# Performance work log

Measured on AMD Instinct MI355X. Metric: run time of the kernel, lower is better.

The kernel has to match this reference:

```python
import jax, jax.numpy as jnp
import numpy as np

M, D, H, E = 4096, 2048, 2048, 8


def q8(t):
    # Emulate fp8 e4m3 quantize->dequantize (DeepGEMM inputs); scale is all-ones in the source.
    return t.astype(jnp.float8_e4m3fn).astype(jnp.float32)


def setup_inputs() -> dict:
    key = jax.random.key(0)
    k1, k2, k3 = jax.random.split(key, 3)
    x = jax.random.normal(k1, (M, D), dtype=jnp.float32)
    gate_w = jax.random.normal(k2, (E, D), dtype=jnp.float32) * (D ** -0.5)
    gate_b = jnp.zeros((E,), dtype=jnp.float32)
    expert_w = jax.random.normal(k3, (E, H, D), dtype=jnp.float32) * (D ** -0.5)
    return {"x": x, "gate_w": gate_w, "gate_b": gate_b, "expert_w": expert_w}


def reference(x, gate_w, gate_b, expert_w):
    # Gating: softmax over experts. [M, E]
    gate_scores = jax.nn.softmax(x @ gate_w.T + gate_b, axis=-1)
    # fp8 quantize-dequantize of activations and expert weights (rhs_scale == 1).
    x_q = q8(x)                      # [M, D]
    w_q = q8(expert_w)               # [E, H, D]
    # Grouped GEMM (every expert applied to every token), bf16 output like deep_gemm.
    y = jnp.einsum("md,ehd->emh", x_q, w_q).astype(jnp.bfloat16)  # [E, M, H]
    # Weighted combine: sum_e gate[m,e] * y[e,m,h]
    out = jnp.einsum("me,emh->mh", gate_scores, y.astype(jnp.float32))  # [M, H]
    return out
```

## Files before the change

kernel.cpp:

```cpp
#include <hip/hip_runtime.h>
#include <hip/hip_bf16.h>

#define MDIM 4096
#define DDIM 2048
#define HDIM 2048
#define EDIM 8
#define HD   ((size_t)HDIM * DDIM)

typedef float v4f __attribute__((ext_vector_type(4)));
typedef int   v4i __attribute__((ext_vector_type(4)));
typedef int   v8i __attribute__((ext_vector_type(8)));

__device__ __forceinline__ void gl2lds16(const void* g, void* l) {
  __builtin_amdgcn_global_load_lds(
      (const __attribute__((address_space(1))) void*)g,
      (__attribute__((address_space(3))) void*)l,
      16, 0, 0);
}

__global__ __launch_bounds__(256) void k_quant(
    const float* __restrict__ x, const float* __restrict__ gw,
    const float* __restrict__ gb, const float* __restrict__ w,
    float* __restrict__ gate, unsigned char* __restrict__ x8,
    unsigned char* __restrict__ w8)
{
  if (blockIdx.x < 1024) {
    const int wid  = threadIdx.x >> 6;
    const int lane = threadIdx.x & 63;
    const int m    = blockIdx.x * 4 + wid;

    const float4* xr = (const float4*)(x + (size_t)m * DDIM);
    unsigned int* qr = (unsigned int*)(x8 + (size_t)m * DDIM);

    float part[EDIM];
#pragma unroll
    for (int e = 0; e < EDIM; ++e) part[e] = 0.f;

#pragma unroll
    for (int it = 0; it < DDIM / 4 / 64; ++it) {
      const int idx = it * 64 + lane;
      const float4 xv = xr[idx];
      int pk = __builtin_amdgcn_cvt_pk_fp8_f32(xv.x, xv.y, 0, false);
      pk = __builtin_amdgcn_cvt_pk_fp8_f32(xv.z, xv.w, pk, true);
      qr[idx] = (unsigned int)pk;
#pragma unroll
      for (int e = 0; e < EDIM; ++e) {
        const float4 wv = ((const float4*)(gw + (size_t)e * DDIM))[idx];
        part[e] += xv.x * wv.x + xv.y * wv.y + xv.z * wv.z + xv.w * wv.w;
      }
    }
#pragma unroll
    for (int e = 0; e < EDIM; ++e) {
#pragma unroll
      for (int off = 32; off > 0; off >>= 1)
        part[e] += __shfl_xor(part[e], off);
    }
    float lg[EDIM];
    float s = 0.f;
#pragma unroll
    for (int e = 0; e < EDIM; ++e) lg[e] = part[e] + gb[e];
    float mx = lg[0];
#pragma unroll
    for (int e = 1; e < EDIM; ++e) mx = fmaxf(mx, lg[e]);
#pragma unroll
    for (int e = 0; e < EDIM; ++e) { lg[e] = expf(lg[e] - mx); s += lg[e]; }
    const float inv = 1.f / s;
    if (lane < EDIM) gate[m * EDIM + lane] = lg[lane] * inv;
  } else {
    const long long n4 = (long long)EDIM * HDIM * DDIM / 4;
    const long long stride = (long long)4096 * 256;
    for (long long i = (long long)(blockIdx.x - 1024) * 256 + threadIdx.x;
         i < n4; i += stride) {
      const float4 v = ((const float4*)w)[i];
      int pk = __builtin_amdgcn_cvt_pk_fp8_f32(v.x, v.y, 0, false);
      pk = __builtin_amdgcn_cvt_pk_fp8_f32(v.z, v.w, pk, true);
      ((unsigned int*)w8)[i] = (unsigned int)pk;
    }
  }
}

__global__ __launch_bounds__(256, 2) void k_moe_gemm(
    const unsigned char* __restrict__ x8,
    const unsigned char* __restrict__ w8,
    const float* __restrict__ gate,
    float* __restrict__ out)
{
  extern __shared__ unsigned char smem[];

  const int tid  = threadIdx.x;
  const int lane = tid & 63;
  const int wid  = tid >> 6;
  const int wm   = wid >> 1;
  const int wn   = wid & 1;

  const int bid   = blockIdx.x;
  const int xcd   = bid & 7;
  const int local = bid >> 3;
  const int tm    = (xcd >> 1) * 8 + (local >> 3);
  const int tn    = (xcd & 1) * 8 + (local & 7);
  const int bm    = tm * 128;
  const int bn    = tn * 128;

  const int lrow = lane & 15;
  const int lk   = lane >> 4;
  const int c0   = (lk * 32) ^ ((lrow & 7) << 4);
  const int c1   = c0 ^ 16;

  const int strow = tid >> 3;
  const int stcol = ((tid & 7) * 16) ^ ((strow & 7) << 4);
  const unsigned char* asrc = x8 + (size_t)(bm + strow) * DDIM + stcol;
  const unsigned char* bsrc = w8 + (size_t)(bn + strow) * DDIM + stcol;

  float* sGf = (float*)(smem + 65536);

  if (tid < 128) {
    const float4 g0 = *(const float4*)(gate + (size_t)(bm + tid) * EDIM);
    const float4 g1 = *(const float4*)(gate + (size_t)(bm + tid) * EDIM + 4);
    sGf[0 * 128 + tid] = g0.x; sGf[1 * 128 + tid] = g0.y;
    sGf[2 * 128 + tid] = g0.z; sGf[3 * 128 + tid] = g0.w;
    sGf[4 * 128 + tid] = g1.x; sGf[5 * 128 + tid] = g1.y;
    sGf[6 * 128 + tid] = g1.z; sGf[7 * 128 + tid] = g1.w;
  }

  v4f acc[4][4];
  v4f outacc[4][4];
#pragma unroll
  for (int i = 0; i < 4; ++i)
#pragma unroll
    for (int j = 0; j < 4; ++j) {
      acc[i][j][0] = 0.f; acc[i][j][1] = 0.f;
      acc[i][j][2] = 0.f; acc[i][j][3] = 0.f;
      outacc[i][j][0] = 0.f; outacc[i][j][1] = 0.f;
      outacc[i][j][2] = 0.f; outacc[i][j][3] = 0.f;
    }

#define STAGE(S) do {                                                          \
    const int    kb_ = ((S) & 15) * 128;                                       \
    const size_t eo_ = (size_t)((S) >> 4) * HD;                                \
    unsigned char* la_ = smem + ((S) & 1) * 16384;                             \
    unsigned char* lb_ = smem + 32768 + ((S) & 1) * 16384;                     \
    _Pragma("unroll") for (int i = 0; i < 4; ++i)                              \
      gl2lds16(asrc + (size_t)i * (32 * DDIM) + kb_,                           \
               (void*)(la_ + i * 4096 + wid * 1024));                          \
    _Pragma("unroll") for (int i = 0; i < 4; ++i)                              \
      gl2lds16(bsrc + eo_ + (size_t)i * (32 * DDIM) + kb_,                     \
               (void*)(lb_ + i * 4096 + wid * 1024));                          \
  } while (0)

#define COMP(S) do {                                                           \
    const unsigned char* pA_ = smem + ((S) & 1) * 16384 +                      \
                               (size_t)(wm * 64 + lrow) * 128;                 \
    const unsigned char* pB_ = smem + 32768 + ((S) & 1) * 16384 +              \
                               (size_t)(wn * 64 + lrow) * 128;                 \
    v8i bv_[4];                                                                \
    _Pragma("unroll") for (int j = 0; j < 4; ++j) {                            \
      union { v8i v; v4i h[2]; } u_;                                           \
      u_.h[0] = *(const v4i*)(pB_ + j * 2048 + c0);                            \
      u_.h[1] = *(const v4i*)(pB_ + j * 2048 + c1);                            \
      bv_[j] = u_.v;                                                           \
    }                                                                          \
    __builtin_amdgcn_s_setprio(1);                                             \
    _Pragma("unroll") for (int i = 0; i < 4; ++i) {                            \
      union { v8i v; v4i h[2]; } ua_;                                          \
      ua_.h[0] = *(const v4i*)(pA_ + i * 2048 + c0);                           \
      ua_.h[1] = *(const v4i*)(pA_ + i * 2048 + c1);                           \
      const v8i av_ = ua_.v;                                                   \
      _Pragma("unroll") for (int j = 0; j < 4; ++j)                            \
        acc[i][j] = __builtin_amdgcn_mfma_scale_f32_16x16x128_f8f6f4(          \
            av_, bv_[j], acc[i][j], 0 , 0 ,                      \
            0, 127 , 0, 127 );                         \
    }                                                                          \
    __builtin_amdgcn_s_setprio(0);                                             \
    if (((S) & 15) == 15) {         \
      const int e_ = (S) >> 4;                                                 \
      _Pragma("unroll") for (int i = 0; i < 4; ++i) {                          \
        const v4f g4_ =                                                        \
            *(const v4f*)(sGf + e_ * 128 + wm * 64 + i * 16 + lk * 4);         \
        _Pragma("unroll") for (int j = 0; j < 4; ++j) {                        \
          outacc[i][j][0] += g4_[0] * acc[i][j][0]; acc[i][j][0] = 0.f;        \
          outacc[i][j][1] += g4_[1] * acc[i][j][1]; acc[i][j][1] = 0.f;        \
          outacc[i][j][2] += g4_[2] * acc[i][j][2]; acc[i][j][2] = 0.f;        \
          outacc[i][j][3] += g4_[3] * acc[i][j][3]; acc[i][j][3] = 0.f;        \
        }                                                                      \
      }                                                                        \
    }                                                                          \
  } while (0)

  STAGE(0);
  __syncthreads();

  for (int s = 0; s < 128; ++s) {
    asm volatile("s_waitcnt vmcnt(0)" ::: "memory");
    __builtin_amdgcn_s_barrier();
    if (s < 127) STAGE(s + 1);
    COMP(s);
  }

#undef COMP
#undef STAGE

#pragma unroll
  for (int i = 0; i < 4; ++i)
#pragma unroll
    for (int q = 0; q < 4; ++q) {
      const size_t r = (size_t)(bm + wm * 64 + i * 16 + lk * 4 + q);
      float* orow = out + r * HDIM + bn + wn * 64 + lrow;
#pragma unroll
      for (int j = 0; j < 4; ++j)
        orow[j * 16] = outacc[i][j][q];
    }
}

extern "C" void kernel_launch(void* const* d_in, const int* in_sizes, int n_in,
                              void* d_out, int out_size, void* d_ws, size_t ws_size,
                              hipStream_t stream) {
  (void)in_sizes; (void)n_in; (void)out_size; (void)ws_size;
  const float* x        = (const float*)d_in[0];
  const float* gate_w   = (const float*)d_in[1];
  const float* gate_b   = (const float*)d_in[2];
  const float* expert_w = (const float*)d_in[3];
  float* out = (float*)d_out;

  char* ws = (char*)d_ws;
  float* gate       = (float*)ws;
  unsigned char* x8 = (unsigned char*)(ws + 131072);
  unsigned char* w8 = (unsigned char*)(ws + 131072 + (size_t)MDIM * DDIM);

  hipLaunchKernelGGL(k_quant, dim3(5120), dim3(256), 0, stream,
                     x, gate_w, gate_b, expert_w, gate, x8, w8);
  hipLaunchKernelGGL(k_moe_gemm, dim3(512), dim3(256), 69632, stream,
                     x8, w8, gate, out);
}
```

Baseline: 159.2 us.

## Load half of B tile directly from global into registers, shrink LDS

Only half of each warp's B columns are now staged through LDS. The other two 16-row B fragments are loaded straight from global memory into registers inside the compute step. This cuts LDS usage from about 68KB to 52KB, which could allow more resident blocks, and it reduces LDS read traffic. MFMA issue is also reordered so that A fragments are preloaded and the instructions are grouped by B column. The risk is that the global loads sit on the critical path, with no prefetch into registers and a possible wait on the vmcnt.

```diff
diff --git a/kernel.cpp b/kernel.cpp
--- a/kernel.cpp
+++ b/kernel.cpp
@@ -111,7 +111,10 @@
   const unsigned char* asrc = x8 + (size_t)(bm + strow) * DDIM + stcol;
   const unsigned char* bsrc = w8 + (size_t)(bn + strow) * DDIM + stcol;
 
-  float* sGf = (float*)(smem + 65536);
+  const unsigned char* bptr =
+      w8 + (size_t)(bn + wn * 64 + lrow) * DDIM + lk * 32;
+
+  float* sGf = (float*)(smem + 48 * 1024);
 
   if (tid < 128) {
     const float4 g0 = *(const float4*)(gate + (size_t)(bm + tid) * EDIM);
@@ -138,41 +141,62 @@
     const int    kb_ = ((S) & 15) * 128;                                       \
     const size_t eo_ = (size_t)((S) >> 4) * HD;                                \
     unsigned char* la_ = smem + ((S) & 1) * 16384;                             \
-    unsigned char* lb_ = smem + 32768 + ((S) & 1) * 16384;                     \
+    unsigned char* lb_ = smem + 32768 + ((S) & 1) * 8192;                      \
     _Pragma("unroll") for (int i = 0; i < 4; ++i)                              \
       gl2lds16(asrc + (size_t)i * (32 * DDIM) + kb_,                           \
                (void*)(la_ + i * 4096 + wid * 1024));                          \
-    _Pragma("unroll") for (int i = 0; i < 4; ++i)                              \
-      gl2lds16(bsrc + eo_ + (size_t)i * (32 * DDIM) + kb_,                     \
+    _Pragma("unroll") for (int i = 0; i < 2; ++i)                              \
+      gl2lds16(bsrc + eo_ + (size_t)i * (64 * DDIM) + kb_,                     \
                (void*)(lb_ + i * 4096 + wid * 1024));                          \
   } while (0)
 
 #define COMP(S) do {                                                           \
+    const int e_ = (S) >> 4;                                                   \
+          \
+    const unsigned char* pb2_ = bptr + (size_t)e_ * HD +                       \
+                                (size_t)(((S) & 15) * 128) +                   \
+                                (size_t)2 * (16 * DDIM);                       \
+    v8i gb2_, gb3_;                                                            \
+    { union { v8i v; v4i h[2]; } u_;                                           \
+      u_.h[0] = *(const v4i*)(pb2_); u_.h[1] = *(const v4i*)(pb2_ + 16);       \
+      gb2_ = u_.v; }                                                           \
+    { const unsigned char* pb3_ = pb2_ + (16 * DDIM);                          \
+      union { v8i v; v4i h[2]; } u_;                                           \
+      u_.h[0] = *(const v4i*)(pb3_); u_.h[1] = *(const v4i*)(pb3_ + 16);       \
+      gb3_ = u_.v; }                                                           \
     const unsigned char* pA_ = smem + ((S) & 1) * 16384 +                      \
                                (size_t)(wm * 64 + lrow) * 128;                 \
-    const unsigned char* pB_ = smem + 32768 + ((S) & 1) * 16384 +              \
-                               (size_t)(wn * 64 + lrow) * 128;                 \
-    v8i bv_[4];                                                                \
-    _Pragma("unroll") for (int j = 0; j < 4; ++j) {                            \
+    const unsigned char* pB_ = smem + 32768 + ((S) & 1) * 8192 +               \
+                               (size_t)(wn * 4096 + lrow * 128);               \
+    v8i bv_[2];                                                                \
+    _Pragma("unroll") for (int j = 0; j < 2; ++j) {                            \
       union { v8i v; v4i h[2]; } u_;                                           \
       u_.h[0] = *(const v4i*)(pB_ + j * 2048 + c0);                            \
       u_.h[1] = *(const v4i*)(pB_ + j * 2048 + c1);                            \
       bv_[j] = u_.v;                                                           \
     }                                                                          \
+    v8i av_[4];                                                                \
+    _Pragma("unroll") for (int i = 0; i < 4; ++i) {                            \
+      union { v8i v; v4i h[2]; } u_;                                           \
+      u_.h[0] = *(const v4i*)(pA_ + i * 2048 + c0);                            \
+      u_.h[1] = *(const v4i*)(pA_ + i * 2048 + c1);                            \
+      av_[i] = u_.v;                                                           \
+    }                                                                          \
     __builtin_amdgcn_s_setprio(1);                                             \
-    _Pragma("unroll") for (int i = 0; i < 4; ++i) {                            \
-      union { v8i v; v4i h[2]; } ua_;                                          \
-      ua_.h[0] = *(const v4i*)(pA_ + i * 2048 + c0);                           \
-      ua_.h[1] = *(const v4i*)(pA_ + i * 2048 + c1);                           \
-      const v8i av_ = ua_.v;                                                   \
-      _Pragma("unroll") for (int j = 0; j < 4; ++j)                            \
-        acc[i][j] = __builtin_amdgcn_mfma_scale_f32_16x16x128_f8f6f4(          \
-            av_, bv_[j], acc[i][j], 0 , 0 ,                      \
-            0, 127 , 0, 127 );                         \
-    }                                                                          \
+    _Pragma("unroll") for (int i = 0; i < 4; ++i)                              \
+      acc[i][0] = __builtin_amdgcn_mfma_scale_f32_16x16x128_f8f6f4(            \
+          av_[i], bv_[0], acc[i][0], 0, 0, 0, 127, 0, 127);                    \
+    _Pragma("unroll") for (int i = 0; i < 4; ++i)                              \
+      acc[i][1] = __builtin_amdgcn_mfma_scale_f32_16x16x128_f8f6f4(            \
+          av_[i], bv_[1], acc[i][1], 0, 0, 0, 127, 0, 127);                    \
+    _Pragma("unroll") for (int i = 0; i < 4; ++i)                              \
+      acc[i][2] = __builtin_amdgcn_mfma_scale_f32_16x16x128_f8f6f4(            \
+          av_[i], gb2_, acc[i][2], 0, 0, 0, 127, 0, 127);                      \
+    _Pragma("unroll") for (int i = 0; i < 4; ++i)                              \
+      acc[i][3] = __builtin_amdgcn_mfma_scale_f32_16x16x128_f8f6f4(            \
+          av_[i], gb3_, acc[i][3], 0, 0, 0, 127, 0, 127);                      \
     __builtin_amdgcn_s_setprio(0);                                             \
     if (((S) & 15) == 15) {         \
-      const int e_ = (S) >> 4;                                                 \
       _Pragma("unroll") for (int i = 0; i < 4; ++i) {                          \
         const v4f g4_ =                                                        \
             *(const v4f*)(sGf + e_ * 128 + wm * 64 + i * 16 + lk * 4);         \
@@ -228,6 +252,6 @@
 
   hipLaunchKernelGGL(k_quant, dim3(5120), dim3(256), 0, stream,
                      x, gate_w, gate_b, expert_w, gate, x8, w8);
-  hipLaunchKernelGGL(k_moe_gemm, dim3(512), dim3(256), 69632, stream,
+  hipLaunchKernelGGL(k_moe_gemm, dim3(512), dim3(256), 53248, stream,
                      x8, w8, gate, out);
 }
```

Measured after the change: 206.2 us. +29.5%, slower.
